# Kernel tuning notes

Measured on AMD Instinct MI355X. Metric: run time of the kernel, lower is better.

The kernel has to match this reference:

```python
import jax, jax.numpy as jnp
import numpy as np

VOXEL_SIZE = 0.05  # init kwarg


def setup_inputs() -> dict:
    key = jax.random.key(0)
    N, B = 4_194_304, 16
    # coords uniform in [0, 5)^3 -> ~100^3 voxel cells per scene at voxel_size=0.05
    coord = jax.random.uniform(key, (N, 3), dtype=jnp.float32) * 5.0
    # cumulative batch offsets (equal-sized scenes), as pointops expects
    offset = (jnp.arange(1, B + 1, dtype=jnp.int32) * (N // B)).astype(jnp.int32)
    return {"coord": coord, "offset": offset}


def _voxel_mean(coord, offset, voxel_size):
    """Faithful jax port of voxelize_helper + segment_csr(mean) + batch2offset.

    Returns:
      n_p    [N,3]  voxel-mean coords, padded with zeros beyond n_voxels
      n_o    [B]    cumulative voxel counts per batch (batch2offset)
      counts [N]    points per voxel (idx_ptr = concat([0], cumsum(counts[valid])))
    """
    N = coord.shape[0]
    B = offset.shape[0]
    # batch id per point from cumulative offsets
    batch = jnp.searchsorted(offset, jnp.arange(N), side='right')  # [N]
    # start = per-batch min coord (start=None path of voxelize_helper)
    start = jax.ops.segment_min(coord, batch, num_segments=B)      # [B,3]
    grid = jnp.floor((coord - start[batch]) / voxel_size).astype(jnp.int32)  # [N,3]
    G = jnp.max(grid) + 1  # grid extent (per-axis upper bound)
    # linearized cluster key: unique per (batch, gx, gy, gz)
    ckey = ((batch * G + grid[:, 0]) * G + grid[:, 1]) * G + grid[:, 2]
    fill = B * G * G * G  # sentinel beyond any real key
    # sorted unique cluster keys == CSR segment order after sorting cluster indices
    uniq, inv = jnp.unique(ckey, return_inverse=True, size=N, fill_value=fill)
    # fused gather + segment-mean (equivalent to coord[sorted_idx] -> segment_csr mean)
    seg_sum = jax.ops.segment_sum(coord, inv, num_segments=N)                 # [N,3]
    counts = jax.ops.segment_sum(jnp.ones((N,), coord.dtype), inv, num_segments=N)
    n_p = seg_sum / jnp.maximum(counts, 1.0)[:, None]
    # batch id per voxel -> batch2offset (cumulative voxel counts)
    valid = uniq < fill
    vbatch = jnp.where(valid, uniq // (G * G * G), B)
    per_batch = jax.ops.segment_sum(valid.astype(jnp.int32), vbatch, num_segments=B + 1)[:B]
    n_o = jnp.cumsum(per_batch)
    return n_p, n_o, counts.astype(jnp.int32)


def reference(coord, offset):
    return _voxel_mean(coord, offset, VOXEL_SIZE)
```

## Files before the change

kernel.cpp:

```cpp
#include <hip/hip_runtime.h>
#include <stdint.h>


typedef unsigned int uint;
typedef unsigned long long u64;

#define VS 0.05f
#define QSCALE (4096.0f / VS)
#define QINV  (VS / 4096.0f)
#define NBUCKET 2048
#define NBLK_P 256
#define DENSE_MAX 8192

__device__ __forceinline__ uint f2m(float f) {
    uint b = __float_as_uint(f);
    return (b & 0x80000000u) ? ~b : (b | 0x80000000u);
}
__device__ __forceinline__ float m2f(uint m) {
    uint b = (m & 0x80000000u) ? (m & 0x7fffffffu) : ~m;
    return __uint_as_float(b);
}

__global__ void k_init(uint* start_m, int B3) {
    int i = blockIdx.x * blockDim.x + threadIdx.x;
    if (i < B3) start_m[i] = 0xFFFFFFFFu;
}

__global__ void __launch_bounds__(256)
k_minmax(const float* __restrict__ coord, const int* __restrict__ offset,
         int N, int B, uint* start_m) {
    __shared__ uint smin[768];
    __shared__ int soff[256];
    int t = threadIdx.x;
    int nb3 = B * 3;
    for (int j = t; j < B; j += 256) soff[j] = offset[j];
    for (int j = t; j < nb3; j += 256) smin[j] = 0xFFFFFFFFu;
    __syncthreads();

    int F = 3 * N;
    int NQ = F >> 2;
    int per = (NQ + gridDim.x - 1) / gridDim.x;
    int qlo = blockIdx.x * per;
    int qhi = min(NQ, qlo + per);
    const float4* __restrict__ c4 = reinterpret_cast<const float4*>(coord);

    bool fast = false;
    int bU = 0;
    if (qlo < qhi) {
        int pF = (4 * qlo) / 3;
        int pL = (4 * qhi - 1) / 3;
        int bF = 0, bL = 0;
        for (int j = 0; j < B; ++j) {
            bF += (pF >= soff[j]) ? 1 : 0;
            bL += (pL >= soff[j]) ? 1 : 0;
        }
        fast = (bF == bL);
        bU = bF;
    }

    if (fast) {
        int q = qlo + t;
        int p0 = q % 3;
        float s0 = INFINITY, s1 = INFINITY, s2 = INFINITY;
        for (;;) {
            if (q >= qhi) break;
            float4 v = c4[q];
            s0 = fminf(s0, fminf(v.x, v.w)); s1 = fminf(s1, v.y); s2 = fminf(s2, v.z);
            q += 256;
            if (q >= qhi) break;
            v = c4[q];
            s1 = fminf(s1, fminf(v.x, v.w)); s2 = fminf(s2, v.y); s0 = fminf(s0, v.z);
            q += 256;
            if (q >= qhi) break;
            v = c4[q];
            s2 = fminf(s2, fminf(v.x, v.w)); s0 = fminf(s0, v.y); s1 = fminf(s1, v.z);
            q += 256;
        }
        float ax, ay, az;
        if (p0 == 0)      { ax = s0; ay = s1; az = s2; }
        else if (p0 == 1) { ax = s2; ay = s0; az = s1; }
        else              { ax = s1; ay = s2; az = s0; }
        for (int d = 32; d; d >>= 1) {
            ax = fminf(ax, __shfl_xor(ax, d));
            ay = fminf(ay, __shfl_xor(ay, d));
            az = fminf(az, __shfl_xor(az, d));
        }
        if ((t & 63) == 0 && ax < INFINITY) {
            atomicMin(&smin[bU * 3 + 0], f2m(ax));
            atomicMin(&smin[bU * 3 + 1], f2m(ay));
            atomicMin(&smin[bU * 3 + 2], f2m(az));
        }
    } else {
        for (int q = qlo + t; q < qhi; q += 256) {
            float4 v = c4[q];
            int e = 4 * q;
            float vals[4] = {v.x, v.y, v.z, v.w};
#pragma unroll
            for (int k = 0; k < 4; ++k) {
                int ee = e + k;
                int pt = ee / 3;
                int axis = ee - 3 * pt;
                int b = 0;
                for (int j = 0; j < B; ++j) b += (pt >= soff[j]) ? 1 : 0;
                atomicMin(&smin[b * 3 + axis], f2m(vals[k]));
            }
        }
    }

    if (blockIdx.x == 0) {
        for (int ee = 4 * NQ + t; ee < F; ee += 256) {
            int pt = ee / 3;
            int axis = ee - 3 * pt;
            int b = 0;
            for (int j = 0; j < B; ++j) b += (pt >= soff[j]) ? 1 : 0;
            atomicMin(&smin[b * 3 + axis], f2m(coord[ee]));
        }
    }
    __syncthreads();
    for (int j = t; j < nb3; j += 256) {
        uint mn = smin[j];
        if (mn != 0xFFFFFFFFu) atomicMin(&start_m[j], mn);
    }
}


__device__ __forceinline__ u64 mk_rec(float x, float y, float z,
                                      float sx, float sy, float sz,
                                      int b, uint& q) {
    int gx = min((int)floorf((x - sx) / VS), 127);
    int gy = min((int)floorf((y - sy) / VS), 127);
    int gz = min((int)floorf((z - sz) / VS), 127);
    float fx = fmaxf(x - (sx + (float)gx * VS), 0.0f);
    float fy = fmaxf(y - (sy + (float)gy * VS), 0.0f);
    float fz = fmaxf(z - (sz + (float)gz * VS), 0.0f);
    uint ux = min((uint)(fx * QSCALE + 0.5f), 4095u);
    uint uy = min((uint)(fy * QSCALE + 0.5f), 4095u);
    uint uz = min((uint)(fz * QSCALE + 0.5f), 4095u);
    uint cell = ((uint)gy << 7) | (uint)gz;
    q = ((uint)b << 7) | (uint)gx;
    return ((u64)q << 50) | ((u64)cell << 36) | ((u64)ux << 24) | ((u64)uy << 12) | (u64)uz;
}

__device__ __forceinline__ void count_point(float x, float y, float z, int b,
                                            float sx, float sy, float sz, int pid,
                                            uint* hist, u64* __restrict__ tmp) {
    uint q;
    u64 rec = mk_rec(x, y, z, sx, sy, sz, b, q);
    atomicAdd(&hist[q], 1u);
    tmp[pid] = rec;
}

__global__ void __launch_bounds__(1024)
k_count3(const float* __restrict__ coord, const int* __restrict__ offset,
         int N, int B, const uint* __restrict__ start_m, uint* __restrict__ histm,
         u64* __restrict__ tmp) {
    __shared__ uint hist[NBUCKET];
    __shared__ int soff[16];
    __shared__ float sstart[48];
    int t = threadIdx.x;
    if (t < B) soff[t] = offset[t];
    if (t < B * 3) sstart[t] = m2f(start_m[t]);
    for (int j = t; j < NBUCKET; j += 1024) hist[j] = 0;
    __syncthreads();
    int chunk = (N + gridDim.x - 1) / gridDim.x;
    int lo = blockIdx.x * chunk, hi = min(N, lo + chunk);
    int bLo = 0, bHi = 0;
    for (int j = 0; j < B; ++j) {
        bLo += (lo >= soff[j]) ? 1 : 0;
        bHi += (hi - 1 >= soff[j]) ? 1 : 0;
    }
    if (lo < hi && bLo == bHi && (lo & 3) == 0) {
        int b = bLo;
        float sx = sstart[b * 3 + 0], sy = sstart[b * 3 + 1], sz = sstart[b * 3 + 2];
        const float4* __restrict__ c4 = reinterpret_cast<const float4*>(coord);
        int gEnd = hi >> 2;
        for (int g = (lo >> 2) + t; g < gEnd; g += 1024) {
            float4 v0 = c4[3 * g], v1 = c4[3 * g + 1], v2 = c4[3 * g + 2];
            int p = 4 * g;
            count_point(v0.x, v0.y, v0.z, b, sx, sy, sz, p + 0, hist, tmp);
            count_point(v0.w, v1.x, v1.y, b, sx, sy, sz, p + 1, hist, tmp);
            count_point(v1.z, v1.w, v2.x, b, sx, sy, sz, p + 2, hist, tmp);
            count_point(v2.y, v2.z, v2.w, b, sx, sy, sz, p + 3, hist, tmp);
        }
        for (int i = (gEnd << 2) + t; i < hi; i += 1024) {
            float x = coord[3 * i + 0], y = coord[3 * i + 1], z = coord[3 * i + 2];
            count_point(x, y, z, b, sx, sy, sz, i, hist, tmp);
        }
    } else {
        for (int i = lo + t; i < hi; i += 1024) {
            float x = coord[3 * i + 0], y = coord[3 * i + 1], z = coord[3 * i + 2];
            int b = 0;
            for (int j = 0; j < B; ++j) b += (i >= soff[j]) ? 1 : 0;
            count_point(x, y, z, b, sstart[b * 3 + 0], sstart[b * 3 + 1],
                        sstart[b * 3 + 2], i, hist, tmp);
        }
    }
    __syncthreads();
    for (int j = t; j < NBUCKET; j += 1024)
        histm[(size_t)j * NBLK_P + blockIdx.x] = hist[j];
}

__global__ void k_scanrow(uint* __restrict__ histm, uint* __restrict__ tot) {
    __shared__ uint sc[256];
    uint* row = histm + (size_t)blockIdx.x * NBLK_P;
    int t = threadIdx.x;
    uint v = row[t];
    sc[t] = v;
    __syncthreads();
    for (int d = 1; d < 256; d <<= 1) {
        uint add = (t >= d) ? sc[t - d] : 0;
        __syncthreads();
        sc[t] += add;
        __syncthreads();
    }
    row[t] = sc[t] - v;
    if (t == 255) tot[blockIdx.x] = sc[255];
}

__global__ void k_scan2048(const uint* __restrict__ in, uint* __restrict__ out) {
    __shared__ uint p[1024];
    int t = threadIdx.x;
    uint a = in[2 * t], bb = in[2 * t + 1];
    p[t] = a + bb;
    __syncthreads();
    for (int d = 1; d < 1024; d <<= 1) {
        uint add = (t >= d) ? p[t - d] : 0;
        __syncthreads();
        p[t] += add;
        __syncthreads();
    }
    uint ex = p[t] - (a + bb);
    out[2 * t] = ex;
    out[2 * t + 1] = ex + a;
    if (t == 1023) out[2048] = p[1023];
}

__global__ void k_scan2048b(const uint* __restrict__ in, uint* __restrict__ out,
                            int B, float* __restrict__ no_out) {
    __shared__ uint p[1024];
    int t = threadIdx.x;
    uint a = in[2 * t], bb = in[2 * t + 1];
    p[t] = a + bb;
    __syncthreads();
    for (int d = 1; d < 1024; d <<= 1) {
        uint add = (t >= d) ? p[t - d] : 0;
        __syncthreads();
        p[t] += add;
        __syncthreads();
    }
    uint ex = p[t] - (a + bb);
    out[2 * t] = ex;
    out[2 * t + 1] = ex + a;
    if (t == 1023) out[2048] = p[1023];
    if (t < B) no_out[t] = (float)p[((t + 1) << 6) - 1];
}

__global__ void __launch_bounds__(1024)
k_scatter(const u64* __restrict__ tmp, int N,
          const uint* __restrict__ histm, const uint* __restrict__ bucket_base,
          u64* __restrict__ recs) {
    __shared__ uint cursor[NBUCKET];
    int t = threadIdx.x;
    for (int j = t; j < NBUCKET; j += 1024)
        cursor[j] = bucket_base[j] + histm[(size_t)j * NBLK_P + blockIdx.x];
    __syncthreads();
    int chunk = (N + gridDim.x - 1) / gridDim.x;
    int lo = blockIdx.x * chunk, hi = min(N, lo + chunk);
    for (int i = lo + t; i < hi; i += 1024) {
        u64 r = tmp[i];
        uint q = (uint)(r >> 50);
        uint slot = atomicAdd(&cursor[q], 1u);
        recs[slot] = r;
    }
}

__global__ void k_vox(const u64* __restrict__ recs, const uint* __restrict__ bucket_base,
                      uint* __restrict__ voxcount, uint* __restrict__ gmask) {
    __shared__ uint bits[512];
    __shared__ uint wsum[4];
    int q = blockIdx.x;
    uint lo = bucket_base[q], hi = bucket_base[q + 1];
    for (int j = threadIdx.x; j < 512; j += blockDim.x) bits[j] = 0;
    __syncthreads();
    for (uint i = lo + threadIdx.x; i < hi; i += blockDim.x) {
        uint c = (uint)(recs[i] >> 36) & 0x3FFFu;
        atomicOr(&bits[c >> 5], 1u << (c & 31));
    }
    __syncthreads();
    uint s = 0;
    for (int w = threadIdx.x; w < 512; w += blockDim.x) {
        uint m = bits[w];
        gmask[(size_t)q * 512 + w] = m;
        s += __popc(m);
    }
    for (int d = 32; d; d >>= 1) s += __shfl_xor(s, d);
    if ((threadIdx.x & 63) == 0) wsum[threadIdx.x >> 6] = s;
    __syncthreads();
    if (threadIdx.x == 0) voxcount[q] = wsum[0] + wsum[1] + wsum[2] + wsum[3];
}

__global__ void __launch_bounds__(1024)
k_emit2(const u64* __restrict__ recs, const uint* __restrict__ bucket_base,
        const uint* __restrict__ voxscan, const uint* __restrict__ gmask,
        const uint* __restrict__ start_m, int N, int B, int out_total,
        float* __restrict__ np_out, float* __restrict__ cnt_out,
        float* __restrict__ out) {
    int t = threadIdx.x;
    if (blockIdx.x >= NBUCKET) {
        uint total = voxscan[NBUCKET];
        int zb = blockIdx.x - NBUCKET;
        int stride = (gridDim.x - NBUCKET) * 1024;
        int tid = zb * 1024 + t;
        for (int j = 3 * (int)total + tid; j < 3 * N; j += stride) np_out[j] = 0.0f;
        for (int j = (int)total + tid; j < N; j += stride) cnt_out[j] = 0.0f;
        for (int j = 4 * N + B + tid; j < out_total; j += stride) out[j] = 0.0f;
        return;
    }
    __shared__ u64 dense[DENSE_MAX];
    __shared__ uint mask[512], wrank[512];
    __shared__ uint wtot[8], woff[9];
    __shared__ float sstart[48];
    int q = blockIdx.x;
    uint lo = bucket_base[q], hi = bucket_base[q + 1];
    if (lo == hi) return;
    if (t < 48) sstart[t] = m2f(start_m[t]);
    uint m = 0, c = 0;
    if (t < 512) {
        m = gmask[(size_t)q * 512 + t];
        mask[t] = m;
        c = __popc(m);
    }
    uint sc = c;
    for (int d = 1; d < 64; d <<= 1) {
        uint nb = __shfl_up(sc, d, 64);
        if ((t & 63) >= d) sc += nb;
    }
    if (t < 512 && (t & 63) == 63) wtot[t >> 6] = sc;
    __syncthreads();
    if (t == 0) {
        uint r = 0;
        for (int k = 0; k < 8; ++k) { woff[k] = r; r += wtot[k]; }
        woff[8] = r;
    }
    __syncthreads();
    if (t < 512) wrank[t] = sc - c + woff[t >> 6];
    uint vc = woff[8];
    uint base_r = voxscan[q];
    int b = q >> 7, gx = q & 127;
    float cx = sstart[b * 3 + 0] + (float)gx * VS;
    float sy = sstart[b * 3 + 1], sz = sstart[b * 3 + 2];
    for (uint segbase = 0; segbase < vc; segbase += DENSE_MAX) {
        uint seglen = min(vc - segbase, (uint)DENSE_MAX);
        for (uint j = t; j < seglen; j += 1024) dense[j] = 0ull;
        __syncthreads();
        for (uint i = lo + t; i < hi; i += 1024) {
            u64 rec = recs[i];
            uint cc = (uint)(rec >> 36) & 0x3FFFu;
            uint w = cc >> 5, bit = cc & 31;
            uint r = wrank[w] + __popc(mask[w] & ((1u << bit) - 1u));
            if (r >= segbase && r < segbase + seglen) {
                u64 enc = (((rec >> 24) & 0xFFFull) << 46) | (((rec >> 12) & 0xFFFull) << 28)
                        | ((rec & 0xFFFull) << 10) | 1ull;
                atomicAdd(&dense[r - segbase], enc);
            }
        }
        __syncthreads();
        for (uint rr = segbase + t; rr < segbase + seglen; rr += 1024) {
            uint l2 = 0, h2 = 511;
            while (l2 < h2) {
                uint mid = (l2 + h2 + 1) >> 1;
                if (wrank[mid] <= rr) l2 = mid; else h2 = mid - 1;
            }
            uint w = l2;
            uint idx = rr - wrank[w];
            uint mm = mask[w], bit = 0, cp;
            cp = __popc(mm & 0xFFFFu); if (idx >= cp) { idx -= cp; bit += 16; mm >>= 16; }
            cp = __popc(mm & 0xFFu);   if (idx >= cp) { idx -= cp; bit += 8;  mm >>= 8; }
            cp = __popc(mm & 0xFu);    if (idx >= cp) { idx -= cp; bit += 4;  mm >>= 4; }
            cp = __popc(mm & 0x3u);    if (idx >= cp) { idx -= cp; bit += 2;  mm >>= 2; }
            cp = __popc(mm & 0x1u);    if (idx >= cp) { bit += 1; }
            uint cell = (w << 5) + bit;
            uint gy = cell >> 7, gz = cell & 127u;
            u64 p = dense[rr - segbase];
            float cnt = (float)(uint)(p & 1023ull);
            float inv = 1.0f / fmaxf(cnt, 1.0f);
            uint uz = (uint)((p >> 10) & 0x3FFFFull);
            uint uy = (uint)((p >> 28) & 0x3FFFFull);
            uint ux = (uint)(p >> 46);
            uint r_out = base_r + rr;
            np_out[3 * r_out + 0] = cx + ((float)ux * QINV) * inv;
            np_out[3 * r_out + 1] = sy + (float)gy * VS + ((float)uy * QINV) * inv;
            np_out[3 * r_out + 2] = sz + (float)gz * VS + ((float)uz * QINV) * inv;
            cnt_out[r_out] = cnt;
        }
        __syncthreads();
    }
}


__device__ __forceinline__ void point_grid(const float* __restrict__ coord, int i,
                                           const int* soff, const float* sstart, int B,
                                           float& x, float& y, float& z,
                                           int& b, int& gx, int& gy, int& gz) {
    x = coord[3 * i + 0]; y = coord[3 * i + 1]; z = coord[3 * i + 2];
    b = 0;
    for (int j = 0; j < B; ++j) b += (i >= soff[j]) ? 1 : 0;
    gx = min((int)floorf((x - sstart[b * 3 + 0]) / VS), 127);
    gy = min((int)floorf((y - sstart[b * 3 + 1]) / VS), 127);
    gz = min((int)floorf((z - sstart[b * 3 + 2]) / VS), 127);
}

__device__ __forceinline__ u64 frac12(float x, float y, float z,
                                      const float* sstart, int b,
                                      int gx, int gy, int gz) {
    float fx = fmaxf(x - (sstart[b * 3 + 0] + (float)gx * VS), 0.0f);
    float fy = fmaxf(y - (sstart[b * 3 + 1] + (float)gy * VS), 0.0f);
    float fz = fmaxf(z - (sstart[b * 3 + 2] + (float)gz * VS), 0.0f);
    uint ux = min((uint)(fx * QSCALE + 0.5f), 4095u);
    uint uy = min((uint)(fy * QSCALE + 0.5f), 4095u);
    uint uz = min((uint)(fz * QSCALE + 0.5f), 4095u);
    return ((u64)ux << 24) | ((u64)uy << 12) | (u64)uz;
}

__global__ void k_hist(const float* __restrict__ coord, const int* __restrict__ offset,
                       int N, int B, const uint* __restrict__ start_m,
                       uint* __restrict__ mask) {
    __shared__ int soff[256];
    __shared__ float sstart[768];
    for (int j = threadIdx.x; j < B; j += blockDim.x) soff[j] = offset[j];
    for (int j = threadIdx.x; j < B * 3; j += blockDim.x) sstart[j] = m2f(start_m[j]);
    __syncthreads();
    int i = blockIdx.x * blockDim.x + threadIdx.x;
    if (i >= N) return;
    float x, y, z; int b, gx, gy, gz;
    point_grid(coord, i, soff, sstart, B, x, y, z, b, gx, gy, gz);
    uint key = ((uint)b << 21) | ((uint)gx << 14) | ((uint)gy << 7) | (uint)gz;
    atomicOr(&mask[key >> 5], 1u << (key & 31));
}

__global__ void k_scan1(const uint* __restrict__ mask, uint* __restrict__ partial) {
    int base = blockIdx.x * 1024 + threadIdx.x * 4;
    uint4 m = *(const uint4*)(mask + base);
    uint s = __popc(m.x) + __popc(m.y) + __popc(m.z) + __popc(m.w);
    for (int d = 32; d; d >>= 1) s += __shfl_xor(s, d);
    __shared__ uint wsum[4];
    if ((threadIdx.x & 63) == 0) wsum[threadIdx.x >> 6] = s;
    __syncthreads();
    if (threadIdx.x == 0) partial[blockIdx.x] = wsum[0] + wsum[1] + wsum[2] + wsum[3];
}

__global__ void k_scan2(uint* partial, int P, uint* total) {
    __shared__ uint t[256];
    uint carry = 0;
    for (int base = 0; base < P; base += 256) {
        int j = base + threadIdx.x;
        uint v = (j < P) ? partial[j] : 0;
        t[threadIdx.x] = v;
        __syncthreads();
        for (int d = 1; d < 256; d <<= 1) {
            uint add = (threadIdx.x >= d) ? t[threadIdx.x - d] : 0;
            __syncthreads();
            t[threadIdx.x] += add;
            __syncthreads();
        }
        uint inc = t[threadIdx.x];
        uint chunk = t[255];
        if (j < P) partial[j] = carry + inc - v;
        __syncthreads();
        carry += chunk;
    }
    if (threadIdx.x == 0) *total = carry;
}

__global__ void k_scan3(const uint* __restrict__ mask, const uint* __restrict__ partial,
                        uint* __restrict__ wordrank) {
    int base = blockIdx.x * 1024 + threadIdx.x * 4;
    uint4 m = *(const uint4*)(mask + base);
    uint c0 = __popc(m.x), c1 = __popc(m.y), c2 = __popc(m.z), c3 = __popc(m.w);
    uint s = c0 + c1 + c2 + c3;
    __shared__ uint t[256];
    t[threadIdx.x] = s;
    __syncthreads();
    for (int d = 1; d < 256; d <<= 1) {
        uint add = (threadIdx.x >= d) ? t[threadIdx.x - d] : 0;
        __syncthreads();
        t[threadIdx.x] += add;
        __syncthreads();
    }
    uint ex = t[threadIdx.x] - s + partial[blockIdx.x];
    uint4 r;
    r.x = ex; r.y = ex + c0; r.z = ex + c0 + c1; r.w = ex + c0 + c1 + c2;
    *(uint4*)(wordrank + base) = r;
}

__global__ void k_no(const uint* mask, const uint* wordrank, const uint* total,
                     float* no_out, int B, int W) {
    int b = blockIdx.x * blockDim.x + threadIdx.x;
    if (b >= B) return;
    long long idx = (long long)(b + 1) << 21;
    uint w = (uint)(idx >> 5);
    uint v;
    if (w >= (uint)W) v = *total;
    else v = wordrank[w];
    no_out[b] = (float)v;
}

__global__ void k_accum_sparse(const float* __restrict__ coord, const int* __restrict__ offset,
                               int N, int B, const uint* __restrict__ start_m,
                               const uint* __restrict__ mask, const uint* __restrict__ wordrank,
                               u64* __restrict__ packed) {
    __shared__ int soff[256];
    __shared__ float sstart[768];
    for (int j = threadIdx.x; j < B; j += blockDim.x) soff[j] = offset[j];
    for (int j = threadIdx.x; j < B * 3; j += blockDim.x) sstart[j] = m2f(start_m[j]);
    __syncthreads();
    int i = blockIdx.x * blockDim.x + threadIdx.x;
    if (i >= N) return;
    float x, y, z; int b, gx, gy, gz;
    point_grid(coord, i, soff, sstart, B, x, y, z, b, gx, gy, gz);
    uint key = ((uint)b << 21) | ((uint)gx << 14) | ((uint)gy << 7) | (uint)gz;
    uint w = key >> 5, bit = key & 31;
    uint r = wordrank[w] + __popc(mask[w] & ((1u << bit) - 1u));
    u64 f = frac12(x, y, z, sstart, b, gx, gy, gz);
    u64 enc = (((f >> 24) & 0xFFFull) << 46) | (((f >> 12) & 0xFFFull) << 28)
            | ((f & 0xFFFull) << 10) | 1ull;
    atomicAdd(&packed[r], enc);
}

__global__ void k_decode_sparse(const uint* __restrict__ mask, const uint* __restrict__ wordrank,
                                const uint* __restrict__ start_m,
                                const u64* __restrict__ packed, int W,
                                float* __restrict__ np_out, float* __restrict__ cnt_out) {
    __shared__ float sstart[48];
    for (int j = threadIdx.x; j < 48; j += blockDim.x) sstart[j] = m2f(start_m[j]);
    __syncthreads();
    int w = blockIdx.x * blockDim.x + threadIdx.x;
    if (w >= W) return;
    uint m = mask[w];
    if (m == 0) return;
    uint r = wordrank[w];
    uint kbase = (uint)w << 5;
    while (m) {
        uint bit = (uint)__ffs(m) - 1u;
        m &= m - 1u;
        uint key = kbase + bit;
        u64 p = packed[r];
        float cnt = (float)(uint)(p & 1023ull);
        float inv = 1.0f / fmaxf(cnt, 1.0f);
        uint uz = (uint)((p >> 10) & 0x3FFFFull);
        uint uy = (uint)((p >> 28) & 0x3FFFFull);
        uint ux = (uint)(p >> 46);
        uint b = key >> 21;
        uint gx = (key >> 14) & 127u;
        uint gy = (key >> 7) & 127u;
        uint gz = key & 127u;
        np_out[3 * r + 0] = sstart[b * 3 + 0] + (float)gx * VS + ((float)ux * QINV) * inv;
        np_out[3 * r + 1] = sstart[b * 3 + 1] + (float)gy * VS + ((float)uy * QINV) * inv;
        np_out[3 * r + 2] = sstart[b * 3 + 2] + (float)gz * VS + ((float)uz * QINV) * inv;
        cnt_out[r] = cnt;
        ++r;
    }
}

extern "C" void kernel_launch(void* const* d_in, const int* in_sizes, int n_in,
                              void* d_out, int out_size, void* d_ws, size_t ws_size,
                              hipStream_t stream) {
    const float* coord = (const float*)d_in[0];
    const int* offset = (const int*)d_in[1];
    int N = in_sizes[0] / 3;
    int B = in_sizes[1];

    float* out = (float*)d_out;
    float* np_out = out;
    float* no_out = out + (size_t)3 * N;
    float* cnt_out = no_out + B;

    uint8_t* base = (uint8_t*)d_ws;
    uint* start_m = (uint*)base;
    uint* total = start_m + (size_t)B * 3;

    uintptr_t p = (uintptr_t)(total + 1);
    p = (p + 255) & ~(uintptr_t)255;
    uint* histm = (uint*)p;          p += (size_t)NBUCKET * NBLK_P * 4;
    p = (p + 255) & ~(uintptr_t)255;
    uint* tot = (uint*)p;            p += (size_t)NBUCKET * 4;
    p = (p + 255) & ~(uintptr_t)255;
    uint* bucket_base = (uint*)p;    p += (size_t)(NBUCKET + 1) * 4;
    p = (p + 255) & ~(uintptr_t)255;
    uint* voxcount = (uint*)p;       p += (size_t)NBUCKET * 4;
    p = (p + 255) & ~(uintptr_t)255;
    uint* voxscan = (uint*)p;        p += (size_t)(NBUCKET + 1) * 4;
    p = (p + 255) & ~(uintptr_t)255;
    uint* gmask = (uint*)p;          p += (size_t)NBUCKET * 512 * 4;
    p = (p + 255) & ~(uintptr_t)255;
    u64* recs = (u64*)p;             p += (size_t)N * 8;
    p = (p + 255) & ~(uintptr_t)255;
    u64* tmp = (u64*)p;              p += (size_t)N * 8;
    size_t need_part = p - (uintptr_t)base;

    k_init<<<(B * 3 + 255) / 256, 256, 0, stream>>>(start_m, B * 3);
    k_minmax<<<2048, 256, 0, stream>>>(coord, offset, N, B, start_m);

    if (B <= 16 && ws_size >= need_part) {
        k_count3<<<NBLK_P, 1024, 0, stream>>>(coord, offset, N, B, start_m, histm, tmp);
        k_scanrow<<<NBUCKET, 256, 0, stream>>>(histm, tot);
        k_scan2048<<<1, 1024, 0, stream>>>(tot, bucket_base);
        k_scatter<<<NBLK_P, 1024, 0, stream>>>(tmp, N, histm, bucket_base, recs);
        k_vox<<<NBUCKET, 256, 0, stream>>>(recs, bucket_base, voxcount, gmask);
        k_scan2048b<<<1, 1024, 0, stream>>>(voxcount, voxscan, B, no_out);
        k_emit2<<<NBUCKET + 1024, 1024, 0, stream>>>(recs, bucket_base, voxscan, gmask,
                                                     start_m, N, B, out_size,
                                                     np_out, cnt_out, out);
    } else {
        hipMemsetAsync(d_out, 0, (size_t)out_size * sizeof(float), stream);
        size_t W = (size_t)B << 16;
        int nblk1 = (int)(W / 1024);
        uintptr_t sp = (uintptr_t)(total + 1);
        sp = (sp + 255) & ~(uintptr_t)255;
        uint* partial = (uint*)sp;   sp += (size_t)nblk1 * 4;
        sp = (sp + 255) & ~(uintptr_t)255;
        uint* mask = (uint*)sp;      sp += W * 4;
        sp = (sp + 255) & ~(uintptr_t)255;
        uint* wordrank = (uint*)sp;  sp += W * 4;
        sp = (sp + 255) & ~(uintptr_t)255;
        u64* packed = (u64*)sp;
        int nb = (N + 255) / 256;
        hipMemsetAsync(mask, 0, W * sizeof(uint), stream);
        hipMemsetAsync(packed, 0, (size_t)N * sizeof(u64), stream);
        k_hist<<<nb, 256, 0, stream>>>(coord, offset, N, B, start_m, mask);
        k_scan1<<<nblk1, 256, 0, stream>>>(mask, partial);
        k_scan2<<<1, 256, 0, stream>>>(partial, nblk1, total);
        k_scan3<<<nblk1, 256, 0, stream>>>(mask, partial, wordrank);
        k_no<<<(B + 63) / 64, 64, 0, stream>>>(mask, wordrank, total, no_out, B, (int)W);
        k_accum_sparse<<<nb, 256, 0, stream>>>(coord, offset, N, B, start_m, mask,
                                               wordrank, packed);
        k_decode_sparse<<<(int)((W + 255) / 256), 256, 0, stream>>>(mask, wordrank, start_m,
                                                                    packed, (int)W,
                                                                    np_out, cnt_out);
    }
}
```

Before: 199.1 us.

## Use wave-shuffle scans and restructure voxel emit with 512-thread blocks

Replaces the shared-memory Hillis-Steele scans in the row and 2048-element scan kernels with wave-level shuffle scans plus a small cross-wave combine, cutting the number of barriers. The emit kernel drops to 512 threads per block with a smaller dense shared buffer, which should let more blocks fit per CU. It also gets a fast path that skips the segment-range check when all voxels fit in one segment. The output phase now walks each mask word's set bits per thread instead of doing a binary search per voxel. The per-word loop can be uneven across threads, and buckets with more voxels than the smaller buffer now need extra segment passes.

```diff
diff --git a/kernel.cpp b/kernel.cpp
--- a/kernel.cpp
+++ b/kernel.cpp
@@ -10,7 +10,7 @@
 #define QINV  (VS / 4096.0f)
 #define NBUCKET 2048
 #define NBLK_P 256
-#define DENSE_MAX 8192
+#define DENSE_MAX 4096
 
 __device__ __forceinline__ uint f2m(float f) {
     uint b = __float_as_uint(f);
@@ -200,59 +200,86 @@
         histm[(size_t)j * NBLK_P + blockIdx.x] = hist[j];
 }
 
-__global__ void k_scanrow(uint* __restrict__ histm, uint* __restrict__ tot) {
-    __shared__ uint sc[256];
+__global__ void __launch_bounds__(256)
+k_scanrow(uint* __restrict__ histm, uint* __restrict__ tot) {
+    __shared__ uint wtot[4], woff[4];
     uint* row = histm + (size_t)blockIdx.x * NBLK_P;
     int t = threadIdx.x;
     uint v = row[t];
-    sc[t] = v;
-    __syncthreads();
-    for (int d = 1; d < 256; d <<= 1) {
-        uint add = (t >= d) ? sc[t - d] : 0;
-        __syncthreads();
-        sc[t] += add;
-        __syncthreads();
-    }
-    row[t] = sc[t] - v;
-    if (t == 255) tot[blockIdx.x] = sc[255];
-}
-
-__global__ void k_scan2048(const uint* __restrict__ in, uint* __restrict__ out) {
-    __shared__ uint p[1024];
+    uint sc = v;
+    for (int d = 1; d < 64; d <<= 1) {
+        uint nb = __shfl_up(sc, d, 64);
+        if ((t & 63) >= d) sc += nb;
+    }
+    if ((t & 63) == 63) wtot[t >> 6] = sc;
+    __syncthreads();
+    if (t == 0) {
+        uint r = 0;
+#pragma unroll
+        for (int k = 0; k < 4; ++k) { woff[k] = r; r += wtot[k]; }
+    }
+    __syncthreads();
+    uint incl = sc + woff[t >> 6];
+    row[t] = incl - v;
+    if (t == 255) tot[blockIdx.x] = incl;
+}
+
+__global__ void __launch_bounds__(1024)
+k_scan2048(const uint* __restrict__ in, uint* __restrict__ out) {
+    __shared__ uint wtot[16], woff[16];
     int t = threadIdx.x;
     uint a = in[2 * t], bb = in[2 * t + 1];
-    p[t] = a + bb;
-    __syncthreads();
-    for (int d = 1; d < 1024; d <<= 1) {
-        uint add = (t >= d) ? p[t - d] : 0;
-        __syncthreads();
-        p[t] += add;
-        __syncthreads();
-    }
-    uint ex = p[t] - (a + bb);
+    uint s = a + bb;
+    uint sc = s;
+    for (int d = 1; d < 64; d <<= 1) {
+        uint nb = __shfl_up(sc, d, 64);
+        if ((t & 63) >= d) sc += nb;
+    }
+    if ((t & 63) == 63) wtot[t >> 6] = sc;
+    __syncthreads();
+    if (t == 0) {
+        uint r = 0;
+#pragma unroll
+        for (int k = 0; k < 16; ++k) { woff[k] = r; r += wtot[k]; }
+    }
+    __syncthreads();
+    uint incl = sc + woff[t >> 6];
+    uint ex = incl - s;
     out[2 * t] = ex;
     out[2 * t + 1] = ex + a;
-    if (t == 1023) out[2048] = p[1023];
-}
-
-__global__ void k_scan2048b(const uint* __restrict__ in, uint* __restrict__ out,
-                            int B, float* __restrict__ no_out) {
-    __shared__ uint p[1024];
+    if (t == 1023) out[2048] = incl;
+}
+
+__global__ void __launch_bounds__(1024)
+k_scan2048b(const uint* __restrict__ in, uint* __restrict__ out,
+            int B, float* __restrict__ no_out) {
+    __shared__ uint wtot[16], woff[16];
     int t = threadIdx.x;
     uint a = in[2 * t], bb = in[2 * t + 1];
-    p[t] = a + bb;
-    __syncthreads();
-    for (int d = 1; d < 1024; d <<= 1) {
-        uint add = (t >= d) ? p[t - d] : 0;
-        __syncthreads();
-        p[t] += add;
-        __syncthreads();
-    }
-    uint ex = p[t] - (a + bb);
+    uint s = a + bb;
+    uint sc = s;
+    for (int d = 1; d < 64; d <<= 1) {
+        uint nb = __shfl_up(sc, d, 64);
+        if ((t & 63) >= d) sc += nb;
+    }
+    if ((t & 63) == 63) wtot[t >> 6] = sc;
+    __syncthreads();
+    if (t == 0) {
+        uint r = 0;
+#pragma unroll
+        for (int k = 0; k < 16; ++k) { woff[k] = r; r += wtot[k]; }
+    }
+    __syncthreads();
+    uint incl = sc + woff[t >> 6];
+    uint ex = incl - s;
     out[2 * t] = ex;
     out[2 * t + 1] = ex + a;
-    if (t == 1023) out[2048] = p[1023];
-    if (t < B) no_out[t] = (float)p[((t + 1) << 6) - 1];
+    if (t == 1023) out[2048] = incl;
+    int tp = t + 1;
+    if ((tp & 63) == 0) {
+        int b = (tp >> 6) - 1;
+        if (b < B) no_out[b] = (float)incl;
+    }
 }
 
 __global__ void __launch_bounds__(1024)
@@ -299,7 +326,7 @@
     if (threadIdx.x == 0) voxcount[q] = wsum[0] + wsum[1] + wsum[2] + wsum[3];
 }
 
-__global__ void __launch_bounds__(1024)
+__global__ void __launch_bounds__(512)
 k_emit2(const u64* __restrict__ recs, const uint* __restrict__ bucket_base,
         const uint* __restrict__ voxscan, const uint* __restrict__ gmask,
         const uint* __restrict__ start_m, int N, int B, int out_total,
@@ -309,8 +336,8 @@
     if (blockIdx.x >= NBUCKET) {
         uint total = voxscan[NBUCKET];
         int zb = blockIdx.x - NBUCKET;
-        int stride = (gridDim.x - NBUCKET) * 1024;
-        int tid = zb * 1024 + t;
+        int stride = (gridDim.x - NBUCKET) * 512;
+        int tid = zb * 512 + t;
         for (int j = 3 * (int)total + tid; j < 3 * N; j += stride) np_out[j] = 0.0f;
         for (int j = (int)total + tid; j < N; j += stride) cnt_out[j] = 0.0f;
         for (int j = 4 * N + B + tid; j < out_total; j += stride) out[j] = 0.0f;
@@ -324,74 +351,82 @@
     uint lo = bucket_base[q], hi = bucket_base[q + 1];
     if (lo == hi) return;
     if (t < 48) sstart[t] = m2f(start_m[t]);
-    uint m = 0, c = 0;
-    if (t < 512) {
-        m = gmask[(size_t)q * 512 + t];
-        mask[t] = m;
-        c = __popc(m);
-    }
+    uint m = gmask[(size_t)q * 512 + t];
+    mask[t] = m;
+    uint c = __popc(m);
     uint sc = c;
     for (int d = 1; d < 64; d <<= 1) {
         uint nb = __shfl_up(sc, d, 64);
         if ((t & 63) >= d) sc += nb;
     }
-    if (t < 512 && (t & 63) == 63) wtot[t >> 6] = sc;
+    if ((t & 63) == 63) wtot[t >> 6] = sc;
     __syncthreads();
     if (t == 0) {
         uint r = 0;
+#pragma unroll
         for (int k = 0; k < 8; ++k) { woff[k] = r; r += wtot[k]; }
         woff[8] = r;
     }
     __syncthreads();
-    if (t < 512) wrank[t] = sc - c + woff[t >> 6];
+    wrank[t] = sc - c + woff[t >> 6];
     uint vc = woff[8];
     uint base_r = voxscan[q];
     int b = q >> 7, gx = q & 127;
     float cx = sstart[b * 3 + 0] + (float)gx * VS;
     float sy = sstart[b * 3 + 1], sz = sstart[b * 3 + 2];
+    bool single = (vc <= (uint)DENSE_MAX);
     for (uint segbase = 0; segbase < vc; segbase += DENSE_MAX) {
         uint seglen = min(vc - segbase, (uint)DENSE_MAX);
-        for (uint j = t; j < seglen; j += 1024) dense[j] = 0ull;
+        for (uint j = t; j < seglen; j += 512) dense[j] = 0ull;
         __syncthreads();
-        for (uint i = lo + t; i < hi; i += 1024) {
-            u64 rec = recs[i];
-            uint cc = (uint)(rec >> 36) & 0x3FFFu;
-            uint w = cc >> 5, bit = cc & 31;
-            uint r = wrank[w] + __popc(mask[w] & ((1u << bit) - 1u));
-            if (r >= segbase && r < segbase + seglen) {
+        if (single) {
+            for (uint i = lo + t; i < hi; i += 512) {
+                u64 rec = recs[i];
+                uint cc = (uint)(rec >> 36) & 0x3FFFu;
+                uint w = cc >> 5, bit = cc & 31;
+                uint r = wrank[w] + __popc(mask[w] & ((1u << bit) - 1u));
                 u64 enc = (((rec >> 24) & 0xFFFull) << 46) | (((rec >> 12) & 0xFFFull) << 28)
                         | ((rec & 0xFFFull) << 10) | 1ull;
-                atomicAdd(&dense[r - segbase], enc);
+                atomicAdd(&dense[r], enc);
             }
+        } else {
+            for (uint i = lo + t; i < hi; i += 512) {
+                u64 rec = recs[i];
+                uint cc = (uint)(rec >> 36) & 0x3FFFu;
+                uint w = cc >> 5, bit = cc & 31;
+                uint r = wrank[w] + __popc(mask[w] & ((1u << bit) - 1u));
+                if (r >= segbase && r < segbase + seglen) {
+                    u64 enc = (((rec >> 24) & 0xFFFull) << 46) | (((rec >> 12) & 0xFFFull) << 28)
+                            | ((rec & 0xFFFull) << 10) | 1ull;
+                    atomicAdd(&dense[r - segbase], enc);
+                }
+            }
         }
         __syncthreads();
-        for (uint rr = segbase + t; rr < segbase + seglen; rr += 1024) {
-            uint l2 = 0, h2 = 511;
-            while (l2 < h2) {
-                uint mid = (l2 + h2 + 1) >> 1;
-                if (wrank[mid] <= rr) l2 = mid; else h2 = mid - 1;
+        {
+            uint mm = mask[t];
+            uint r = wrank[t];
+            uint kbase = (uint)t << 5;
+            while (mm) {
+                uint bit = (uint)__ffs(mm) - 1u;
+                mm &= mm - 1u;
+                if (r >= segbase && r < segbase + seglen) {
+                    uint cell = kbase + bit;
+                    uint gy = cell >> 7, gz = cell & 127u;
+                    u64 p = dense[r - segbase];
+                    float cnt = (float)(uint)(p & 1023ull);
+                    float inv = 1.0f / fmaxf(cnt, 1.0f);
+                    uint uz = (uint)((p >> 10) & 0x3FFFFull);
+                    uint uy = (uint)((p >> 28) & 0x3FFFFull);
+                    uint ux = (uint)(p >> 46);
+                    uint r_out = base_r + r;
+                    np_out[3 * r_out + 0] = cx + ((float)ux * QINV) * inv;
+                    np_out[3 * r_out + 1] = sy + (float)gy * VS + ((float)uy * QINV) * inv;
+                    np_out[3 * r_out + 2] = sz + (float)gz * VS + ((float)uz * QINV) * inv;
+                    cnt_out[r_out] = cnt;
+                }
+                ++r;
             }
-            uint w = l2;
-            uint idx = rr - wrank[w];
-            uint mm = mask[w], bit = 0, cp;
-            cp = __popc(mm & 0xFFFFu); if (idx >= cp) { idx -= cp; bit += 16; mm >>= 16; }
-            cp = __popc(mm & 0xFFu);   if (idx >= cp) { idx -= cp; bit += 8;  mm >>= 8; }
-            cp = __popc(mm & 0xFu);    if (idx >= cp) { idx -= cp; bit += 4;  mm >>= 4; }
-            cp = __popc(mm & 0x3u);    if (idx >= cp) { idx -= cp; bit += 2;  mm >>= 2; }
-            cp = __popc(mm & 0x1u);    if (idx >= cp) { bit += 1; }
-            uint cell = (w << 5) + bit;
-            uint gy = cell >> 7, gz = cell & 127u;
-            u64 p = dense[rr - segbase];
-            float cnt = (float)(uint)(p & 1023ull);
-            float inv = 1.0f / fmaxf(cnt, 1.0f);
-            uint uz = (uint)((p >> 10) & 0x3FFFFull);
-            uint uy = (uint)((p >> 28) & 0x3FFFFull);
-            uint ux = (uint)(p >> 46);
-            uint r_out = base_r + rr;
-            np_out[3 * r_out + 0] = cx + ((float)ux * QINV) * inv;
-            np_out[3 * r_out + 1] = sy + (float)gy * VS + ((float)uy * QINV) * inv;
-            np_out[3 * r_out + 2] = sz + (float)gz * VS + ((float)uz * QINV) * inv;
-            cnt_out[r_out] = cnt;
         }
         __syncthreads();
     }
@@ -608,9 +643,9 @@
         k_scatter<<<NBLK_P, 1024, 0, stream>>>(tmp, N, histm, bucket_base, recs);
         k_vox<<<NBUCKET, 256, 0, stream>>>(recs, bucket_base, voxcount, gmask);
         k_scan2048b<<<1, 1024, 0, stream>>>(voxcount, voxscan, B, no_out);
-        k_emit2<<<NBUCKET + 1024, 1024, 0, stream>>>(recs, bucket_base, voxscan, gmask,
-                                                     start_m, N, B, out_size,
-                                                     np_out, cnt_out, out);
+        k_emit2<<<NBUCKET + 1024, 512, 0, stream>>>(recs, bucket_base, voxscan, gmask,
+                                                    start_m, N, B, out_size,
+                                                    np_out, cnt_out, out);
     } else {
         hipMemsetAsync(d_out, 0, (size_t)out_size * sizeof(float), stream);
         size_t W = (size_t)B << 16;
```

Result: slower. 237.9 us (+19.5%).

## Fold single-block prefix-scan kernels into consumers using wave-shuffle scans

Applied to the files above, without the earlier changes.

Removes the two single-block 2048-element scan kernels. Each consumer block (scatter, vox, emit) now recomputes the prefix offsets it needs from the per-bucket totals, using wave shuffles and redundant reductions, and emit's block 0 writes the per-batch voxel offsets. The row scan also switches from a shared-memory Hillis-Steele loop to a wave-shuffle scan. This cuts two serialized kernel launches and their sync-heavy scans, at the cost of redundant reads of the totals array from L2 in every block.

```diff
diff --git a/kernel.cpp b/kernel.cpp
--- a/kernel.cpp
+++ b/kernel.cpp
@@ -200,69 +200,55 @@
         histm[(size_t)j * NBLK_P + blockIdx.x] = hist[j];
 }
 
-__global__ void k_scanrow(uint* __restrict__ histm, uint* __restrict__ tot) {
-    __shared__ uint sc[256];
+__global__ void __launch_bounds__(256)
+k_scanrow(uint* __restrict__ histm, uint* __restrict__ tot) {
+    __shared__ uint wtot[4], woff[4];
     uint* row = histm + (size_t)blockIdx.x * NBLK_P;
     int t = threadIdx.x;
     uint v = row[t];
-    sc[t] = v;
-    __syncthreads();
-    for (int d = 1; d < 256; d <<= 1) {
-        uint add = (t >= d) ? sc[t - d] : 0;
-        __syncthreads();
-        sc[t] += add;
-        __syncthreads();
-    }
-    row[t] = sc[t] - v;
-    if (t == 255) tot[blockIdx.x] = sc[255];
-}
-
-__global__ void k_scan2048(const uint* __restrict__ in, uint* __restrict__ out) {
-    __shared__ uint p[1024];
-    int t = threadIdx.x;
-    uint a = in[2 * t], bb = in[2 * t + 1];
-    p[t] = a + bb;
-    __syncthreads();
-    for (int d = 1; d < 1024; d <<= 1) {
-        uint add = (t >= d) ? p[t - d] : 0;
-        __syncthreads();
-        p[t] += add;
-        __syncthreads();
-    }
-    uint ex = p[t] - (a + bb);
-    out[2 * t] = ex;
-    out[2 * t + 1] = ex + a;
-    if (t == 1023) out[2048] = p[1023];
-}
-
-__global__ void k_scan2048b(const uint* __restrict__ in, uint* __restrict__ out,
-                            int B, float* __restrict__ no_out) {
-    __shared__ uint p[1024];
-    int t = threadIdx.x;
-    uint a = in[2 * t], bb = in[2 * t + 1];
-    p[t] = a + bb;
-    __syncthreads();
-    for (int d = 1; d < 1024; d <<= 1) {
-        uint add = (t >= d) ? p[t - d] : 0;
-        __syncthreads();
-        p[t] += add;
-        __syncthreads();
-    }
-    uint ex = p[t] - (a + bb);
-    out[2 * t] = ex;
-    out[2 * t + 1] = ex + a;
-    if (t == 1023) out[2048] = p[1023];
-    if (t < B) no_out[t] = (float)p[((t + 1) << 6) - 1];
+    uint sc = v;
+    for (int d = 1; d < 64; d <<= 1) {
+        uint nb = __shfl_up(sc, d, 64);
+        if ((t & 63) >= d) sc += nb;
+    }
+    if ((t & 63) == 63) wtot[t >> 6] = sc;
+    __syncthreads();
+    if (t == 0) {
+        uint r = 0;
+#pragma unroll
+        for (int k = 0; k < 4; ++k) { woff[k] = r; r += wtot[k]; }
+    }
+    __syncthreads();
+    uint incl = sc + woff[t >> 6];
+    row[t] = incl - v;
+    if (t == 255) tot[blockIdx.x] = incl;
 }
 
 __global__ void __launch_bounds__(1024)
 k_scatter(const u64* __restrict__ tmp, int N,
-          const uint* __restrict__ histm, const uint* __restrict__ bucket_base,
+          const uint* __restrict__ histm, const uint* __restrict__ tot,
           u64* __restrict__ recs) {
     __shared__ uint cursor[NBUCKET];
+    __shared__ uint wtot[16], woff[16];
     int t = threadIdx.x;
-    for (int j = t; j < NBUCKET; j += 1024)
-        cursor[j] = bucket_base[j] + histm[(size_t)j * NBLK_P + blockIdx.x];
+    uint a = tot[2 * t], bb = tot[2 * t + 1];
+    uint s = a + bb, sc = s;
+    for (int d = 1; d < 64; d <<= 1) {
+        uint nb = __shfl_up(sc, d, 64);
+        if ((t & 63) >= d) sc += nb;
+    }
+    if ((t & 63) == 63) wtot[t >> 6] = sc;
+    __syncthreads();
+    if (t == 0) {
+        uint r = 0;
+#pragma unroll
+        for (int k = 0; k < 16; ++k) { woff[k] = r; r += wtot[k]; }
+    }
+    __syncthreads();
+    uint incl = sc + woff[t >> 6];
+    uint ex = incl - s;
+    cursor[2 * t] = ex + histm[(size_t)(2 * t) * NBLK_P + blockIdx.x];
+    cursor[2 * t + 1] = ex + a + histm[(size_t)(2 * t + 1) * NBLK_P + blockIdx.x];
     __syncthreads();
     int chunk = (N + gridDim.x - 1) / gridDim.x;
     int lo = blockIdx.x * chunk, hi = min(N, lo + chunk);
@@ -274,40 +260,57 @@
     }
 }
 
-__global__ void k_vox(const u64* __restrict__ recs, const uint* __restrict__ bucket_base,
-                      uint* __restrict__ voxcount, uint* __restrict__ gmask) {
+__global__ void __launch_bounds__(256)
+k_vox(const u64* __restrict__ recs, const uint* __restrict__ tot,
+      uint* __restrict__ voxcount, uint* __restrict__ gmask) {
     __shared__ uint bits[512];
     __shared__ uint wsum[4];
+    __shared__ uint shlo;
     int q = blockIdx.x;
-    uint lo = bucket_base[q], hi = bucket_base[q + 1];
-    for (int j = threadIdx.x; j < 512; j += blockDim.x) bits[j] = 0;
-    __syncthreads();
-    for (uint i = lo + threadIdx.x; i < hi; i += blockDim.x) {
+    int t = threadIdx.x;
+    uint s1 = 0;
+    for (int j = t; j < q; j += 256) s1 += tot[j];
+    for (int d = 32; d; d >>= 1) s1 += __shfl_xor(s1, d);
+    if ((t & 63) == 0) wsum[t >> 6] = s1;
+    bits[t] = 0;
+    bits[t + 256] = 0;
+    __syncthreads();
+    if (t == 0) shlo = wsum[0] + wsum[1] + wsum[2] + wsum[3];
+    __syncthreads();
+    uint lo = shlo, hi = lo + tot[q];
+    for (uint i = lo + t; i < hi; i += 256) {
         uint c = (uint)(recs[i] >> 36) & 0x3FFFu;
         atomicOr(&bits[c >> 5], 1u << (c & 31));
     }
     __syncthreads();
-    uint s = 0;
-    for (int w = threadIdx.x; w < 512; w += blockDim.x) {
-        uint m = bits[w];
-        gmask[(size_t)q * 512 + w] = m;
-        s += __popc(m);
-    }
+    uint m0 = bits[t], m1 = bits[t + 256];
+    gmask[(size_t)q * 512 + t] = m0;
+    gmask[(size_t)q * 512 + t + 256] = m1;
+    uint s = __popc(m0) + __popc(m1);
     for (int d = 32; d; d >>= 1) s += __shfl_xor(s, d);
-    if ((threadIdx.x & 63) == 0) wsum[threadIdx.x >> 6] = s;
-    __syncthreads();
-    if (threadIdx.x == 0) voxcount[q] = wsum[0] + wsum[1] + wsum[2] + wsum[3];
+    if ((t & 63) == 0) wsum[t >> 6] = s;
+    __syncthreads();
+    if (t == 0) voxcount[q] = wsum[0] + wsum[1] + wsum[2] + wsum[3];
 }
 
 __global__ void __launch_bounds__(1024)
-k_emit2(const u64* __restrict__ recs, const uint* __restrict__ bucket_base,
-        const uint* __restrict__ voxscan, const uint* __restrict__ gmask,
+k_emit2(const u64* __restrict__ recs, const uint* __restrict__ tot,
+        const uint* __restrict__ voxcount, const uint* __restrict__ gmask,
         const uint* __restrict__ start_m, int N, int B, int out_total,
-        float* __restrict__ np_out, float* __restrict__ cnt_out,
-        float* __restrict__ out) {
+        float* __restrict__ np_out, float* __restrict__ no_out,
+        float* __restrict__ cnt_out, float* __restrict__ out) {
     int t = threadIdx.x;
     if (blockIdx.x >= NBUCKET) {
-        uint total = voxscan[NBUCKET];
+        __shared__ uint wred[16];
+        __shared__ uint totsh;
+        uint s = 0;
+        for (int j = t; j < NBUCKET; j += 1024) s += voxcount[j];
+        for (int d = 32; d; d >>= 1) s += __shfl_xor(s, d);
+        if ((t & 63) == 0) wred[t >> 6] = s;
+        __syncthreads();
+        if (t == 0) { uint r = 0; for (int k = 0; k < 16; ++k) r += wred[k]; totsh = r; }
+        __syncthreads();
+        uint total = totsh;
         int zb = blockIdx.x - NBUCKET;
         int stride = (gridDim.x - NBUCKET) * 1024;
         int tid = zb * 1024 + t;
@@ -318,10 +321,42 @@
     }
     __shared__ u64 dense[DENSE_MAX];
     __shared__ uint mask[512], wrank[512];
-    __shared__ uint wtot[8], woff[9];
+    __shared__ uint wtot[16], woff[17];
     __shared__ float sstart[48];
+    __shared__ uint shlo, shbase;
     int q = blockIdx.x;
-    uint lo = bucket_base[q], hi = bucket_base[q + 1];
+    uint s1 = 0, s2 = 0;
+    for (int j = t; j < q; j += 1024) { s1 += tot[j]; s2 += voxcount[j]; }
+    for (int d = 32; d; d >>= 1) { s1 += __shfl_xor(s1, d); s2 += __shfl_xor(s2, d); }
+    if ((t & 63) == 0) { wtot[t >> 6] = s1; woff[t >> 6] = s2; }
+    __syncthreads();
+    if (t == 0) {
+        uint r1 = 0, r2 = 0;
+        for (int k = 0; k < 16; ++k) { r1 += wtot[k]; r2 += woff[k]; }
+        shlo = r1; shbase = r2;
+    }
+    __syncthreads();
+    uint lo = shlo, hi = lo + tot[q];
+    uint base_r = shbase;
+    if (q == 0) {
+        uint a = voxcount[2 * t], bb = voxcount[2 * t + 1];
+        uint sp = a + bb, scn = sp;
+        for (int d = 1; d < 64; d <<= 1) {
+            uint nb = __shfl_up(scn, d, 64);
+            if ((t & 63) >= d) scn += nb;
+        }
+        if ((t & 63) == 63) wtot[t >> 6] = scn;
+        __syncthreads();
+        if (t == 0) { uint r = 0; for (int k = 0; k < 16; ++k) { woff[k] = r; r += wtot[k]; } }
+        __syncthreads();
+        uint incl = scn + woff[t >> 6];
+        int tp = t + 1;
+        if ((tp & 63) == 0) {
+            int b = (tp >> 6) - 1;
+            if (b < B) no_out[b] = (float)incl;
+        }
+        __syncthreads();
+    }
     if (lo == hi) return;
     if (t < 48) sstart[t] = m2f(start_m[t]);
     uint m = 0, c = 0;
@@ -345,7 +380,6 @@
     __syncthreads();
     if (t < 512) wrank[t] = sc - c + woff[t >> 6];
     uint vc = woff[8];
-    uint base_r = voxscan[q];
     int b = q >> 7, gx = q & 127;
     float cx = sstart[b * 3 + 0] + (float)gx * VS;
     float sy = sstart[b * 3 + 1], sz = sstart[b * 3 + 2];
@@ -585,11 +619,7 @@
     p = (p + 255) & ~(uintptr_t)255;
     uint* tot = (uint*)p;            p += (size_t)NBUCKET * 4;
     p = (p + 255) & ~(uintptr_t)255;
-    uint* bucket_base = (uint*)p;    p += (size_t)(NBUCKET + 1) * 4;
-    p = (p + 255) & ~(uintptr_t)255;
     uint* voxcount = (uint*)p;       p += (size_t)NBUCKET * 4;
-    p = (p + 255) & ~(uintptr_t)255;
-    uint* voxscan = (uint*)p;        p += (size_t)(NBUCKET + 1) * 4;
     p = (p + 255) & ~(uintptr_t)255;
     uint* gmask = (uint*)p;          p += (size_t)NBUCKET * 512 * 4;
     p = (p + 255) & ~(uintptr_t)255;
@@ -604,13 +634,11 @@
     if (B <= 16 && ws_size >= need_part) {
         k_count3<<<NBLK_P, 1024, 0, stream>>>(coord, offset, N, B, start_m, histm, tmp);
         k_scanrow<<<NBUCKET, 256, 0, stream>>>(histm, tot);
-        k_scan2048<<<1, 1024, 0, stream>>>(tot, bucket_base);
-        k_scatter<<<NBLK_P, 1024, 0, stream>>>(tmp, N, histm, bucket_base, recs);
-        k_vox<<<NBUCKET, 256, 0, stream>>>(recs, bucket_base, voxcount, gmask);
-        k_scan2048b<<<1, 1024, 0, stream>>>(voxcount, voxscan, B, no_out);
-        k_emit2<<<NBUCKET + 1024, 1024, 0, stream>>>(recs, bucket_base, voxscan, gmask,
+        k_scatter<<<NBLK_P, 1024, 0, stream>>>(tmp, N, histm, tot, recs);
+        k_vox<<<NBUCKET, 256, 0, stream>>>(recs, tot, voxcount, gmask);
+        k_emit2<<<NBUCKET + 1024, 1024, 0, stream>>>(recs, tot, voxcount, gmask,
                                                      start_m, N, B, out_size,
-                                                     np_out, cnt_out, out);
+                                                     np_out, no_out, cnt_out, out);
     } else {
         hipMemsetAsync(d_out, 0, (size_t)out_size * sizeof(float), stream);
         size_t W = (size_t)B << 16;
```

After: 201.3 us. About the same (+1.1%).
